# Kernel tuning notes

Measured on AMD Instinct MI355X. Metric: run time of the kernel, lower is better.

## Reference

```python
import jax, jax.numpy as jnp
import numpy as np

DILATION = 3
HC_MULT = 4
HIDDEN_DIM = 32
ENGRAM_DIM = 32
KERNEL_SIZE = 4
EPS = 1.1920929e-07  # torch RMSNorm default eps=None -> finfo(fp32).eps


def rmsnorm(x, w):
    # x: [..., C], w broadcastable to x
    ms = jnp.mean(x * x, axis=-1, keepdims=True)
    return x * jax.lax.rsqrt(ms + EPS) * w


def setup_inputs() -> dict:
    key = jax.random.key(0)
    ks = jax.random.split(key, 12)
    B, T = 16, 8192
    s = 0.05
    return {
        "embeddings": jax.random.normal(ks[0], (B, T, ENGRAM_DIM), jnp.float32),
        "hidden_states": jax.random.normal(ks[1], (B, T, HC_MULT, HIDDEN_DIM), jnp.float32),
        "Wv": jax.random.normal(ks[2], (HIDDEN_DIM, ENGRAM_DIM), jnp.float32) * s,
        "bv": jax.random.normal(ks[3], (HIDDEN_DIM,), jnp.float32) * s,
        "Wk": jax.random.normal(ks[4], (HC_MULT, HIDDEN_DIM, ENGRAM_DIM), jnp.float32) * s,
        "bk": jax.random.normal(ks[5], (HC_MULT, HIDDEN_DIM), jnp.float32) * s,
        "n1_w": jnp.ones((HC_MULT, HIDDEN_DIM), jnp.float32),
        "n2_w": jnp.ones((HC_MULT, HIDDEN_DIM), jnp.float32),
        "cn_w": jnp.ones((HC_MULT, HIDDEN_DIM), jnp.float32),
        "conv_w": jax.random.normal(ks[6], (HC_MULT * HIDDEN_DIM, 1, KERNEL_SIZE), jnp.float32) * s,
    }


def reference(embeddings, hidden_states, Wv, bv, Wk, bk, n1_w, n2_w, cn_w, conv_w):
    B, T, G, C = hidden_states.shape
    # per-branch key projection: [B,T,G,C]
    key = jnp.einsum("btd,gcd->btgc", embeddings, Wk) + bk
    normed_key = rmsnorm(key, n1_w)                    # [B,T,G,C]
    normed_query = rmsnorm(hidden_states, n2_w)        # [B,T,G,C]
    gate = jnp.sum(normed_key * normed_query, axis=-1) / np.sqrt(C)  # [B,T,G]
    gate = jnp.sqrt(jnp.maximum(jnp.abs(gate), 1e-6)) * jnp.sign(gate)
    gate = jax.nn.sigmoid(gate)[..., None]             # [B,T,G,1]
    value = (embeddings @ Wv.T + bv)[:, :, None, :]    # [B,T,1,C]
    gated = gate * value                               # [B,T,G,C]
    # per-branch RMSNorm then concat channels
    x_norm = rmsnorm(gated, cn_w).reshape(B, T, G * C)
    x_bct = jnp.transpose(x_norm, (0, 2, 1))           # [B, G*C, T]
    pad = (KERNEL_SIZE - 1) * DILATION                 # causal left pad = 9
    y_bct = jax.lax.conv_general_dilated(
        x_bct, conv_w,
        window_strides=(1,), padding=[(pad, 0)],
        rhs_dilation=(DILATION,),
        dimension_numbers=("NCH", "OIH", "NCH"),
        feature_group_count=G * C,
    )
    y_bct = jax.nn.silu(y_bct)
    conv_out = jnp.transpose(y_bct, (0, 2, 1)).reshape(B, T, G, C)
    return gated + conv_out
```

## Files before the change

kernel.cpp:

```cpp
#include <hip/hip_runtime.h>
#include <hip/hip_fp16.h>

#define TT    64
#define HALO  9
#define NTOK  73
#define XSTR  132
#define VSTR  36
#define EPS   1.1920929e-07f

typedef __attribute__((ext_vector_type(8))) _Float16 f16x8;
typedef __attribute__((ext_vector_type(4))) float f32x4;

template<int CTRL>
__device__ __forceinline__ float dpp_add(float x) {
    int y = __builtin_amdgcn_update_dpp(0, __float_as_int(x), CTRL, 0xF, 0xF, true);
    return x + __int_as_float(y);
}
__device__ __forceinline__ float redsum16(float x) {
    x = dpp_add<0x128>(x);
    x = dpp_add<0x124>(x);
    x = dpp_add<0x122>(x);
    x = dpp_add<0x121>(x);
    return x;
}

__device__ __forceinline__ float fast_rcp(float x) {
    return __builtin_amdgcn_rcpf(x);
}

extern "C" __global__ __launch_bounds__(320, 3)
void engram_fused(const float* __restrict__ emb,
                  const float* __restrict__ hid,
                  const float* __restrict__ Wv,
                  const float* __restrict__ bv,
                  const float* __restrict__ Wk,
                  const float* __restrict__ bk,
                  const float* __restrict__ n1w,
                  const float* __restrict__ n2w,
                  const float* __restrict__ cnw,
                  const float* __restrict__ cw,
                  float* __restrict__ out)
{
    __shared__ __align__(16) __half s_xn[NTOK * XSTR];
    __shared__ __align__(16) float  s_val[TT * VSTR];
    __shared__ float  s_gate[TT * 4];

    const int tid  = threadIdx.x;
    const int b    = blockIdx.x >> 7;
    const int tile = blockIdx.x & 127;
    const int t0   = tile * TT;

    const int wv  = tid >> 6;
    const int ln  = tid & 63;
    const int l15 = ln & 15;
    const int q   = ln >> 4;
    const int ibase = wv * 16 + q * 4;


    float2 q2[4][4];
    float  okm[4];
    #pragma unroll
    for (int r = 0; r < 4; ++r) {
        int t = t0 - HALO + ibase + r;
        okm[r] = (t >= 0 && t < 8192) ? 1.f : 0.f;
        int tc = t < 0 ? 0 : (t > 8191 ? 8191 : t);
        const float2* qp = (const float2*)&hid[(size_t)((b << 13) + tc) * 128];
        #pragma unroll
        for (int g = 0; g < 4; ++g) q2[r][g] = qp[g * 16 + l15];
    }

    float4 f0, f1;
    float amask;
    {
        const int tA = t0 - HALO + wv * 16 + l15;
        amask = (tA >= 0 && tA < 8192) ? 1.f : 0.f;
        const int tAc = tA < 0 ? 0 : (tA > 8191 ? 8191 : tA);
        const float4* p = (const float4*)&emb[(size_t)((b << 13) + tAc) * 32 + q * 8];
        f0 = p[0];
        f1 = p[1];
    }

    const float2 bv2 = ((const float2*)bv)[l15];
    float2 bk2[4], wn1[4], wn2[4], wcn[4];
    #pragma unroll
    for (int g = 0; g < 4; ++g) {
        bk2[g] = ((const float2*)(bk  + g * 32))[l15];
        wn1[g] = ((const float2*)(n1w + g * 32))[l15];
        wn2[g] = ((const float2*)(n2w + g * 32))[l15];
        wcn[g] = ((const float2*)(cnw + g * 32))[l15];
    }

    f16x8 a;
    a[0] = (_Float16)(amask * f0.x); a[1] = (_Float16)(amask * f0.y);
    a[2] = (_Float16)(amask * f0.z); a[3] = (_Float16)(amask * f0.w);
    a[4] = (_Float16)(amask * f1.x); a[5] = (_Float16)(amask * f1.y);
    a[6] = (_Float16)(amask * f1.z); a[7] = (_Float16)(amask * f1.w);

    f32x4 D[10];
    #pragma unroll
    for (int nt = 0; nt < 10; ++nt) {
        const int e = nt & 1, p = nt >> 1;
        const int ch = 2 * l15 + e;
        const float* wrow = (p == 0) ? &Wv[ch * 32] : &Wk[((p - 1) * 32 + ch) * 32];
        float4 w0 = ((const float4*)wrow)[q * 2];
        float4 w1 = ((const float4*)wrow)[q * 2 + 1];
        f16x8 bf;
        bf[0] = (_Float16)w0.x; bf[1] = (_Float16)w0.y;
        bf[2] = (_Float16)w0.z; bf[3] = (_Float16)w0.w;
        bf[4] = (_Float16)w1.x; bf[5] = (_Float16)w1.y;
        bf[6] = (_Float16)w1.z; bf[7] = (_Float16)w1.w;
        const float bias = (p == 0) ? (e ? bv2.y : bv2.x)
                                    : (e ? bk2[p - 1].y : bk2[p - 1].x);
        f32x4 c = {bias, bias, bias, bias};
        D[nt] = __builtin_amdgcn_mfma_f32_16x16x32_f16(a, bf, c, 0, 0, 0);
    }

    #pragma unroll
    for (int r = 0; r < 4; ++r) {
        const int i = ibase + r;
        const float V0 = D[0][r], V1 = D[1][r];
        float msv = redsum16(V0 * V0 + V1 * V1);
        float gs[4];
        float xn[4][2];
        #pragma unroll
        for (int g = 0; g < 4; ++g) {
            const float K0 = D[2 + 2 * g][r], K1 = D[3 + 2 * g][r];
            const float q0 = q2[r][g].x * okm[r], q1 = q2[r][g].y * okm[r];
            float msk = redsum16(K0 * K0 + K1 * K1);
            float msq = redsum16(q0 * q0 + q1 * q1);
            float dr  = redsum16(K0 * wn1[g].x * q0 * wn2[g].x
                               + K1 * wn1[g].y * q1 * wn2[g].y);
            float rk = rsqrtf(msk * (1.f / 32.f) + EPS);
            float rq = rsqrtf(msq * (1.f / 32.f) + EPS);
            float dot = dr * rk * rq * 0.17677669529663689f;
            float sa = sqrtf(fmaxf(fabsf(dot), 1e-6f));
            float gate = fast_rcp(1.f + __expf(-copysignf(sa, dot)));
            gs[g] = gate;
            float sc = gate * rsqrtf(gate * gate * msv * (1.f / 32.f) + EPS);
            xn[g][0] = sc * V0 * wcn[g].x;
            xn[g][1] = sc * V1 * wcn[g].y;
        }
        if (i < NTOK) {
            #pragma unroll
            for (int g = 0; g < 4; ++g) {
                __half2 h2 = __floats2half2_rn(okm[r] * xn[g][0], okm[r] * xn[g][1]);
                *(__half2*)&s_xn[i * XSTR + g * 32 + 2 * l15] = h2;
            }
            if (i >= HALO) {
                const int j = i - HALO;
                *(float2*)&s_val[j * VSTR + 2 * l15] = make_float2(V0, V1);
                if (l15 < 4) {
                    float gsel = (l15 == 0) ? gs[0] : (l15 == 1) ? gs[1]
                               : (l15 == 2) ? gs[2] : gs[3];
                    s_gate[j * 4 + l15] = gsel;
                }
            }
        }
    }
    __syncthreads();

    const float4* cw4p = (const float4*)cw;
    for (int idx = tid; idx < TT * 32; idx += 320) {
        const int j  = idx >> 5;
        const int c4 = (idx & 31) << 2;
        float4 w0 = cw4p[c4 + 0];
        float4 w1 = cw4p[c4 + 1];
        float4 w2 = cw4p[c4 + 2];
        float4 w3 = cw4p[c4 + 3];
        float y0 = 0.f, y1 = 0.f, y2 = 0.f, y3 = 0.f;
        #pragma unroll
        for (int k = 0; k < 4; ++k) {
            const __half2* xp = (const __half2*)&s_xn[(j + 3 * k) * XSTR + c4];
            float2 a01 = __half22float2(xp[0]);
            float2 a23 = __half22float2(xp[1]);
            const float wk0 = (k == 0) ? w0.x : (k == 1) ? w0.y : (k == 2) ? w0.z : w0.w;
            const float wk1 = (k == 0) ? w1.x : (k == 1) ? w1.y : (k == 2) ? w1.z : w1.w;
            const float wk2 = (k == 0) ? w2.x : (k == 1) ? w2.y : (k == 2) ? w2.z : w2.w;
            const float wk3 = (k == 0) ? w3.x : (k == 1) ? w3.y : (k == 2) ? w3.z : w3.w;
            y0 = fmaf(a01.x, wk0, y0);
            y1 = fmaf(a01.y, wk1, y1);
            y2 = fmaf(a23.x, wk2, y2);
            y3 = fmaf(a23.y, wk3, y3);
        }
        const float g  = s_gate[j * 4 + (c4 >> 5)];
        const f32x4 v  = *(const f32x4*)&s_val[j * VSTR + (c4 & 31)];
        float4 o;
        o.x = g * v[0] + y0 * fast_rcp(1.f + __expf(-y0));
        o.y = g * v[1] + y1 * fast_rcp(1.f + __expf(-y1));
        o.z = g * v[2] + y2 * fast_rcp(1.f + __expf(-y2));
        o.w = g * v[3] + y3 * fast_rcp(1.f + __expf(-y3));
        *(float4*)&out[(size_t)((b << 13) + t0 + j) * 128 + c4] = o;
    }
}

extern "C" void kernel_launch(void* const* d_in, const int* in_sizes, int n_in,
                              void* d_out, int out_size, void* d_ws, size_t ws_size,
                              hipStream_t stream) {
    const float* emb = (const float*)d_in[0];
    const float* hid = (const float*)d_in[1];
    const float* Wv  = (const float*)d_in[2];
    const float* bvp = (const float*)d_in[3];
    const float* Wk  = (const float*)d_in[4];
    const float* bkp = (const float*)d_in[5];
    const float* n1  = (const float*)d_in[6];
    const float* n2  = (const float*)d_in[7];
    const float* cn  = (const float*)d_in[8];
    const float* cwp = (const float*)d_in[9];
    float* out = (float*)d_out;

    dim3 grid(16 * 128);
    dim3 block(320);
    engram_fused<<<grid, block, 0, stream>>>(emb, hid, Wv, bvp, Wk, bkp, n1, n2, cn, cwp, out);
}
```

Baseline: 191.2 us.

## Keep gate and value in registers; compute conv epilogue in MFMA lane layout

Drops the shared-memory staging of the value vector and per-token gates. The conv+SiLU epilogue now runs in the same thread/token mapping as the MFMA accumulators, so gate and value are read straight from registers. Launch bounds are raised to target six blocks per CU. The cost is that some lanes (halo rows) sit idle in the epilogue, outputs become float2 stores instead of float4, and register pressure under the tighter launch bound may cause spills.

Measured after the change: 235.9 us. +23.4%, slower.

```diff
diff --git a/kernel.cpp b/kernel.cpp
--- a/kernel.cpp
+++ b/kernel.cpp
@@ -5,7 +5,6 @@
 #define HALO  9
 #define NTOK  73
 #define XSTR  132
-#define VSTR  36
 #define EPS   1.1920929e-07f
 
 typedef __attribute__((ext_vector_type(8))) _Float16 f16x8;
@@ -28,7 +27,7 @@
     return __builtin_amdgcn_rcpf(x);
 }
 
-extern "C" __global__ __launch_bounds__(320, 3)
+extern "C" __global__ __launch_bounds__(320, 6)
 void engram_fused(const float* __restrict__ emb,
                   const float* __restrict__ hid,
                   const float* __restrict__ Wv,
@@ -42,8 +41,6 @@
                   float* __restrict__ out)
 {
     __shared__ __align__(16) __half s_xn[NTOK * XSTR];
-    __shared__ __align__(16) float  s_val[TT * VSTR];
-    __shared__ float  s_gate[TT * 4];
 
     const int tid  = threadIdx.x;
     const int b    = blockIdx.x >> 7;
@@ -115,12 +112,12 @@
         D[nt] = __builtin_amdgcn_mfma_f32_16x16x32_f16(a, bf, c, 0, 0, 0);
     }
 
+    float gs4[4][4];
     #pragma unroll
     for (int r = 0; r < 4; ++r) {
         const int i = ibase + r;
         const float V0 = D[0][r], V1 = D[1][r];
         float msv = redsum16(V0 * V0 + V1 * V1);
-        float gs[4];
         float xn[4][2];
         #pragma unroll
         for (int g = 0; g < 4; ++g) {
@@ -135,7 +132,7 @@
             float dot = dr * rk * rq * 0.17677669529663689f;
             float sa = sqrtf(fmaxf(fabsf(dot), 1e-6f));
             float gate = fast_rcp(1.f + __expf(-copysignf(sa, dot)));
-            gs[g] = gate;
+            gs4[r][g] = gate;
             float sc = gate * rsqrtf(gate * gate * msv * (1.f / 32.f) + EPS);
             xn[g][0] = sc * V0 * wcn[g].x;
             xn[g][1] = sc * V1 * wcn[g].y;
@@ -146,50 +143,40 @@
                 __half2 h2 = __floats2half2_rn(okm[r] * xn[g][0], okm[r] * xn[g][1]);
                 *(__half2*)&s_xn[i * XSTR + g * 32 + 2 * l15] = h2;
             }
-            if (i >= HALO) {
-                const int j = i - HALO;
-                *(float2*)&s_val[j * VSTR + 2 * l15] = make_float2(V0, V1);
-                if (l15 < 4) {
-                    float gsel = (l15 == 0) ? gs[0] : (l15 == 1) ? gs[1]
-                               : (l15 == 2) ? gs[2] : gs[3];
-                    s_gate[j * 4 + l15] = gsel;
+        }
+    }
+    __syncthreads();
+
+    const float4* cw4p = (const float4*)cw;
+    #pragma unroll
+    for (int g = 0; g < 4; ++g) {
+        const int ch = g * 32 + 2 * l15;
+        const float4 wA = cw4p[ch];
+        const float4 wB = cw4p[ch + 1];
+        #pragma unroll
+        for (int r = 0; r < 4; ++r) {
+            const int i = ibase + r;
+            const int j = i - HALO;
+            if (i >= HALO && i < NTOK) {
+                float y0 = 0.f, y1 = 0.f;
+                #pragma unroll
+                for (int k = 0; k < 4; ++k) {
+                    float2 x = __half22float2(
+                        *(const __half2*)&s_xn[(j + 3 * k) * XSTR + ch]);
+                    const float wk0 = (k == 0) ? wA.x : (k == 1) ? wA.y
+                                    : (k == 2) ? wA.z : wA.w;
+                    const float wk1 = (k == 0) ? wB.x : (k == 1) ? wB.y
+                                    : (k == 2) ? wB.z : wB.w;
+                    y0 = fmaf(x.x, wk0, y0);
+                    y1 = fmaf(x.y, wk1, y1);
                 }
+                const float gg = gs4[r][g];
+                float2 o;
+                o.x = gg * D[0][r] + y0 * fast_rcp(1.f + __expf(-y0));
+                o.y = gg * D[1][r] + y1 * fast_rcp(1.f + __expf(-y1));
+                *(float2*)&out[(size_t)((b << 13) + t0 + j) * 128 + ch] = o;
             }
         }
-    }
-    __syncthreads();
-
-    const float4* cw4p = (const float4*)cw;
-    for (int idx = tid; idx < TT * 32; idx += 320) {
-        const int j  = idx >> 5;
-        const int c4 = (idx & 31) << 2;
-        float4 w0 = cw4p[c4 + 0];
-        float4 w1 = cw4p[c4 + 1];
-        float4 w2 = cw4p[c4 + 2];
-        float4 w3 = cw4p[c4 + 3];
-        float y0 = 0.f, y1 = 0.f, y2 = 0.f, y3 = 0.f;
-        #pragma unroll
-        for (int k = 0; k < 4; ++k) {
-            const __half2* xp = (const __half2*)&s_xn[(j + 3 * k) * XSTR + c4];
-            float2 a01 = __half22float2(xp[0]);
-            float2 a23 = __half22float2(xp[1]);
-            const float wk0 = (k == 0) ? w0.x : (k == 1) ? w0.y : (k == 2) ? w0.z : w0.w;
-            const float wk1 = (k == 0) ? w1.x : (k == 1) ? w1.y : (k == 2) ? w1.z : w1.w;
-            const float wk2 = (k == 0) ? w2.x : (k == 1) ? w2.y : (k == 2) ? w2.z : w2.w;
-            const float wk3 = (k == 0) ? w3.x : (k == 1) ? w3.y : (k == 2) ? w3.z : w3.w;
-            y0 = fmaf(a01.x, wk0, y0);
-            y1 = fmaf(a01.y, wk1, y1);
-            y2 = fmaf(a23.x, wk2, y2);
-            y3 = fmaf(a23.y, wk3, y3);
-        }
-        const float g  = s_gate[j * 4 + (c4 >> 5)];
-        const f32x4 v  = *(const f32x4*)&s_val[j * VSTR + (c4 & 31)];
-        float4 o;
-        o.x = g * v[0] + y0 * fast_rcp(1.f + __expf(-y0));
-        o.y = g * v[1] + y1 * fast_rcp(1.f + __expf(-y1));
-        o.z = g * v[2] + y2 * fast_rcp(1.f + __expf(-y2));
-        o.w = g * v[3] + y3 * fast_rcp(1.f + __expf(-y3));
-        *(float4*)&out[(size_t)((b << 13) + t0 + j) * 128 + c4] = o;
     }
 }
 
```

## Process two time tiles per block and prefetch next tile's hidden states

Applied to the files above, without the earlier changes.

Each block now handles two consecutive 64-token sub-tiles in a loop, with the grid halved. The hidden-state loads for the second sub-tile are issued before the first sub-tile's conv/output phase, so their latency overlaps that work. It also amortises per-block setup (bias and norm weight loads) over two tiles. In exchange it adds register pressure from a second q2 buffer, an extra barrier, and fewer blocks in flight, which can lower occupancy and the latency hiding it provides.

Result: slower. 225.8 us (+18.1%).

```diff
diff --git a/kernel.cpp b/kernel.cpp
--- a/kernel.cpp
+++ b/kernel.cpp
@@ -2,6 +2,7 @@
 #include <hip/hip_fp16.h>
 
 #define TT    64
+#define NSUB  2
 #define HALO  9
 #define NTOK  73
 #define XSTR  132
@@ -46,39 +47,14 @@
     __shared__ float  s_gate[TT * 4];
 
     const int tid  = threadIdx.x;
-    const int b    = blockIdx.x >> 7;
-    const int tile = blockIdx.x & 127;
-    const int t0   = tile * TT;
+    const int b    = blockIdx.x >> 6;
+    const int tp   = blockIdx.x & 63;
 
     const int wv  = tid >> 6;
     const int ln  = tid & 63;
     const int l15 = ln & 15;
     const int q   = ln >> 4;
     const int ibase = wv * 16 + q * 4;
-
-
-    float2 q2[4][4];
-    float  okm[4];
-    #pragma unroll
-    for (int r = 0; r < 4; ++r) {
-        int t = t0 - HALO + ibase + r;
-        okm[r] = (t >= 0 && t < 8192) ? 1.f : 0.f;
-        int tc = t < 0 ? 0 : (t > 8191 ? 8191 : t);
-        const float2* qp = (const float2*)&hid[(size_t)((b << 13) + tc) * 128];
-        #pragma unroll
-        for (int g = 0; g < 4; ++g) q2[r][g] = qp[g * 16 + l15];
-    }
-
-    float4 f0, f1;
-    float amask;
-    {
-        const int tA = t0 - HALO + wv * 16 + l15;
-        amask = (tA >= 0 && tA < 8192) ? 1.f : 0.f;
-        const int tAc = tA < 0 ? 0 : (tA > 8191 ? 8191 : tA);
-        const float4* p = (const float4*)&emb[(size_t)((b << 13) + tAc) * 32 + q * 8];
-        f0 = p[0];
-        f1 = p[1];
-    }
 
     const float2 bv2 = ((const float2*)bv)[l15];
     float2 bk2[4], wn1[4], wn2[4], wcn[4];
@@ -90,106 +66,162 @@
         wcn[g] = ((const float2*)(cnw + g * 32))[l15];
     }
 
-    f16x8 a;
-    a[0] = (_Float16)(amask * f0.x); a[1] = (_Float16)(amask * f0.y);
-    a[2] = (_Float16)(amask * f0.z); a[3] = (_Float16)(amask * f0.w);
-    a[4] = (_Float16)(amask * f1.x); a[5] = (_Float16)(amask * f1.y);
-    a[6] = (_Float16)(amask * f1.z); a[7] = (_Float16)(amask * f1.w);
-
-    f32x4 D[10];
+    float2 q2[4][4];
+    float  okm[4];
+    {
+        const int t0 = tp * (TT * NSUB);
+        #pragma unroll
+        for (int r = 0; r < 4; ++r) {
+            int t = t0 - HALO + ibase + r;
+            okm[r] = (t >= 0 && t < 8192) ? 1.f : 0.f;
+            int tc = t < 0 ? 0 : (t > 8191 ? 8191 : t);
+            const float2* qp = (const float2*)&hid[(size_t)((b << 13) + tc) * 128];
+            #pragma unroll
+            for (int g = 0; g < 4; ++g) q2[r][g] = qp[g * 16 + l15];
+        }
+    }
+
     #pragma unroll
-    for (int nt = 0; nt < 10; ++nt) {
-        const int e = nt & 1, p = nt >> 1;
-        const int ch = 2 * l15 + e;
-        const float* wrow = (p == 0) ? &Wv[ch * 32] : &Wk[((p - 1) * 32 + ch) * 32];
-        float4 w0 = ((const float4*)wrow)[q * 2];
-        float4 w1 = ((const float4*)wrow)[q * 2 + 1];
-        f16x8 bf;
-        bf[0] = (_Float16)w0.x; bf[1] = (_Float16)w0.y;
-        bf[2] = (_Float16)w0.z; bf[3] = (_Float16)w0.w;
-        bf[4] = (_Float16)w1.x; bf[5] = (_Float16)w1.y;
-        bf[6] = (_Float16)w1.z; bf[7] = (_Float16)w1.w;
-        const float bias = (p == 0) ? (e ? bv2.y : bv2.x)
-                                    : (e ? bk2[p - 1].y : bk2[p - 1].x);
-        f32x4 c = {bias, bias, bias, bias};
-        D[nt] = __builtin_amdgcn_mfma_f32_16x16x32_f16(a, bf, c, 0, 0, 0);
-    }
-
-    #pragma unroll
-    for (int r = 0; r < 4; ++r) {
-        const int i = ibase + r;
-        const float V0 = D[0][r], V1 = D[1][r];
-        float msv = redsum16(V0 * V0 + V1 * V1);
-        float gs[4];
-        float xn[4][2];
+    for (int sub = 0; sub < NSUB; ++sub) {
+        const int t0 = tp * (TT * NSUB) + sub * TT;
+
+        float4 f0, f1;
+        float amask;
+        {
+            const int tA = t0 - HALO + wv * 16 + l15;
+            amask = (tA >= 0 && tA < 8192) ? 1.f : 0.f;
+            const int tAc = tA < 0 ? 0 : (tA > 8191 ? 8191 : tA);
+            const float4* p = (const float4*)&emb[(size_t)((b << 13) + tAc) * 32 + q * 8];
+            f0 = p[0];
+            f1 = p[1];
+        }
+
+        f16x8 a;
+        a[0] = (_Float16)(amask * f0.x); a[1] = (_Float16)(amask * f0.y);
+        a[2] = (_Float16)(amask * f0.z); a[3] = (_Float16)(amask * f0.w);
+        a[4] = (_Float16)(amask * f1.x); a[5] = (_Float16)(amask * f1.y);
+        a[6] = (_Float16)(amask * f1.z); a[7] = (_Float16)(amask * f1.w);
+
+        f32x4 D[10];
         #pragma unroll
-        for (int g = 0; g < 4; ++g) {
-            const float K0 = D[2 + 2 * g][r], K1 = D[3 + 2 * g][r];
-            const float q0 = q2[r][g].x * okm[r], q1 = q2[r][g].y * okm[r];
-            float msk = redsum16(K0 * K0 + K1 * K1);
-            float msq = redsum16(q0 * q0 + q1 * q1);
-            float dr  = redsum16(K0 * wn1[g].x * q0 * wn2[g].x
-                               + K1 * wn1[g].y * q1 * wn2[g].y);
-            float rk = rsqrtf(msk * (1.f / 32.f) + EPS);
-            float rq = rsqrtf(msq * (1.f / 32.f) + EPS);
-            float dot = dr * rk * rq * 0.17677669529663689f;
-            float sa = sqrtf(fmaxf(fabsf(dot), 1e-6f));
-            float gate = fast_rcp(1.f + __expf(-copysignf(sa, dot)));
-            gs[g] = gate;
-            float sc = gate * rsqrtf(gate * gate * msv * (1.f / 32.f) + EPS);
-            xn[g][0] = sc * V0 * wcn[g].x;
-            xn[g][1] = sc * V1 * wcn[g].y;
-        }
-        if (i < NTOK) {
+        for (int nt = 0; nt < 10; ++nt) {
+            const int e = nt & 1, p = nt >> 1;
+            const int ch = 2 * l15 + e;
+            const float* wrow = (p == 0) ? &Wv[ch * 32] : &Wk[((p - 1) * 32 + ch) * 32];
+            float4 w0 = ((const float4*)wrow)[q * 2];
+            float4 w1 = ((const float4*)wrow)[q * 2 + 1];
+            f16x8 bf;
+            bf[0] = (_Float16)w0.x; bf[1] = (_Float16)w0.y;
+            bf[2] = (_Float16)w0.z; bf[3] = (_Float16)w0.w;
+            bf[4] = (_Float16)w1.x; bf[5] = (_Float16)w1.y;
+            bf[6] = (_Float16)w1.z; bf[7] = (_Float16)w1.w;
+            const float bias = (p == 0) ? (e ? bv2.y : bv2.x)
+                                        : (e ? bk2[p - 1].y : bk2[p - 1].x);
+            f32x4 c = {bias, bias, bias, bias};
+            D[nt] = __builtin_amdgcn_mfma_f32_16x16x32_f16(a, bf, c, 0, 0, 0);
+        }
+
+        #pragma unroll
+        for (int r = 0; r < 4; ++r) {
+            const int i = ibase + r;
+            const float V0 = D[0][r], V1 = D[1][r];
+            float msv = redsum16(V0 * V0 + V1 * V1);
+            float gs[4];
+            float xn[4][2];
             #pragma unroll
             for (int g = 0; g < 4; ++g) {
-                __half2 h2 = __floats2half2_rn(okm[r] * xn[g][0], okm[r] * xn[g][1]);
-                *(__half2*)&s_xn[i * XSTR + g * 32 + 2 * l15] = h2;
-            }
-            if (i >= HALO) {
-                const int j = i - HALO;
-                *(float2*)&s_val[j * VSTR + 2 * l15] = make_float2(V0, V1);
-                if (l15 < 4) {
-                    float gsel = (l15 == 0) ? gs[0] : (l15 == 1) ? gs[1]
-                               : (l15 == 2) ? gs[2] : gs[3];
-                    s_gate[j * 4 + l15] = gsel;
+                const float K0 = D[2 + 2 * g][r], K1 = D[3 + 2 * g][r];
+                const float q0 = q2[r][g].x * okm[r], q1 = q2[r][g].y * okm[r];
+                float msk = redsum16(K0 * K0 + K1 * K1);
+                float msq = redsum16(q0 * q0 + q1 * q1);
+                float dr  = redsum16(K0 * wn1[g].x * q0 * wn2[g].x
+                                   + K1 * wn1[g].y * q1 * wn2[g].y);
+                float rk = rsqrtf(msk * (1.f / 32.f) + EPS);
+                float rq = rsqrtf(msq * (1.f / 32.f) + EPS);
+                float dot = dr * rk * rq * 0.17677669529663689f;
+                float sa = sqrtf(fmaxf(fabsf(dot), 1e-6f));
+                float gate = fast_rcp(1.f + __expf(-copysignf(sa, dot)));
+                gs[g] = gate;
+                float sc = gate * rsqrtf(gate * gate * msv * (1.f / 32.f) + EPS);
+                xn[g][0] = sc * V0 * wcn[g].x;
+                xn[g][1] = sc * V1 * wcn[g].y;
+            }
+            if (i < NTOK) {
+                #pragma unroll
+                for (int g = 0; g < 4; ++g) {
+                    __half2 h2 = __floats2half2_rn(okm[r] * xn[g][0], okm[r] * xn[g][1]);
+                    *(__half2*)&s_xn[i * XSTR + g * 32 + 2 * l15] = h2;
                 }
-            }
-        }
-    }
-    __syncthreads();
-
-    const float4* cw4p = (const float4*)cw;
-    for (int idx = tid; idx < TT * 32; idx += 320) {
-        const int j  = idx >> 5;
-        const int c4 = (idx & 31) << 2;
-        float4 w0 = cw4p[c4 + 0];
-        float4 w1 = cw4p[c4 + 1];
-        float4 w2 = cw4p[c4 + 2];
-        float4 w3 = cw4p[c4 + 3];
-        float y0 = 0.f, y1 = 0.f, y2 = 0.f, y3 = 0.f;
-        #pragma unroll
-        for (int k = 0; k < 4; ++k) {
-            const __half2* xp = (const __half2*)&s_xn[(j + 3 * k) * XSTR + c4];
-            float2 a01 = __half22float2(xp[0]);
-            float2 a23 = __half22float2(xp[1]);
-            const float wk0 = (k == 0) ? w0.x : (k == 1) ? w0.y : (k == 2) ? w0.z : w0.w;
-            const float wk1 = (k == 0) ? w1.x : (k == 1) ? w1.y : (k == 2) ? w1.z : w1.w;
-            const float wk2 = (k == 0) ? w2.x : (k == 1) ? w2.y : (k == 2) ? w2.z : w2.w;
-            const float wk3 = (k == 0) ? w3.x : (k == 1) ? w3.y : (k == 2) ? w3.z : w3.w;
-            y0 = fmaf(a01.x, wk0, y0);
-            y1 = fmaf(a01.y, wk1, y1);
-            y2 = fmaf(a23.x, wk2, y2);
-            y3 = fmaf(a23.y, wk3, y3);
-        }
-        const float g  = s_gate[j * 4 + (c4 >> 5)];
-        const f32x4 v  = *(const f32x4*)&s_val[j * VSTR + (c4 & 31)];
-        float4 o;
-        o.x = g * v[0] + y0 * fast_rcp(1.f + __expf(-y0));
-        o.y = g * v[1] + y1 * fast_rcp(1.f + __expf(-y1));
-        o.z = g * v[2] + y2 * fast_rcp(1.f + __expf(-y2));
-        o.w = g * v[3] + y3 * fast_rcp(1.f + __expf(-y3));
-        *(float4*)&out[(size_t)((b << 13) + t0 + j) * 128 + c4] = o;
+                if (i >= HALO) {
+                    const int j = i - HALO;
+                    *(float2*)&s_val[j * VSTR + 2 * l15] = make_float2(V0, V1);
+                    if (l15 < 4) {
+                        float gsel = (l15 == 0) ? gs[0] : (l15 == 1) ? gs[1]
+                                   : (l15 == 2) ? gs[2] : gs[3];
+                        s_gate[j * 4 + l15] = gsel;
+                    }
+                }
+            }
+        }
+        __syncthreads();
+
+        float2 q2n[4][4];
+        float  okmn[4];
+        if (sub + 1 < NSUB) {
+            const int t0n = t0 + TT;
+            #pragma unroll
+            for (int r = 0; r < 4; ++r) {
+                int t = t0n - HALO + ibase + r;
+                okmn[r] = (t >= 0 && t < 8192) ? 1.f : 0.f;
+                int tc = t < 0 ? 0 : (t > 8191 ? 8191 : t);
+                const float2* qp = (const float2*)&hid[(size_t)((b << 13) + tc) * 128];
+                #pragma unroll
+                for (int g = 0; g < 4; ++g) q2n[r][g] = qp[g * 16 + l15];
+            }
+        }
+
+        const float4* cw4p = (const float4*)cw;
+        for (int idx = tid; idx < TT * 32; idx += 320) {
+            const int j  = idx >> 5;
+            const int c4 = (idx & 31) << 2;
+            float4 w0 = cw4p[c4 + 0];
+            float4 w1 = cw4p[c4 + 1];
+            float4 w2 = cw4p[c4 + 2];
+            float4 w3 = cw4p[c4 + 3];
+            float y0 = 0.f, y1 = 0.f, y2 = 0.f, y3 = 0.f;
+            #pragma unroll
+            for (int k = 0; k < 4; ++k) {
+                const __half2* xp = (const __half2*)&s_xn[(j + 3 * k) * XSTR + c4];
+                float2 a01 = __half22float2(xp[0]);
+                float2 a23 = __half22float2(xp[1]);
+                const float wk0 = (k == 0) ? w0.x : (k == 1) ? w0.y : (k == 2) ? w0.z : w0.w;
+                const float wk1 = (k == 0) ? w1.x : (k == 1) ? w1.y : (k == 2) ? w1.z : w1.w;
+                const float wk2 = (k == 0) ? w2.x : (k == 1) ? w2.y : (k == 2) ? w2.z : w2.w;
+                const float wk3 = (k == 0) ? w3.x : (k == 1) ? w3.y : (k == 2) ? w3.z : w3.w;
+                y0 = fmaf(a01.x, wk0, y0);
+                y1 = fmaf(a01.y, wk1, y1);
+                y2 = fmaf(a23.x, wk2, y2);
+                y3 = fmaf(a23.y, wk3, y3);
+            }
+            const float g  = s_gate[j * 4 + (c4 >> 5)];
+            const f32x4 v  = *(const f32x4*)&s_val[j * VSTR + (c4 & 31)];
+            float4 o;
+            o.x = g * v[0] + y0 * fast_rcp(1.f + __expf(-y0));
+            o.y = g * v[1] + y1 * fast_rcp(1.f + __expf(-y1));
+            o.z = g * v[2] + y2 * fast_rcp(1.f + __expf(-y2));
+            o.w = g * v[3] + y3 * fast_rcp(1.f + __expf(-y3));
+            *(float4*)&out[(size_t)((b << 13) + t0 + j) * 128 + c4] = o;
+        }
+
+        if (sub + 1 < NSUB) {
+            #pragma unroll
+            for (int r = 0; r < 4; ++r) {
+                okm[r] = okmn[r];
+                #pragma unroll
+                for (int g = 0; g < 4; ++g) q2[r][g] = q2n[r][g];
+            }
+            __syncthreads();
+        }
     }
 }
 
@@ -208,7 +240,7 @@
     const float* cwp = (const float*)d_in[9];
     float* out = (float*)d_out;
 
-    dim3 grid(16 * 128);
+    dim3 grid(16 * 64);
     dim3 block(320);
     engram_fused<<<grid, block, 0, stream>>>(emb, hid, Wv, bvp, Wk, bkp, n1, n2, cn, cwp, out);
 }
```

## Split fused kernel into norm and conv kernels via workspace

Applied to the files above, without the earlier changes.

Splits the single fused kernel into two. The first computes projections, gates and normalized activations per token and writes them to a global workspace (fp16 xn, fp32 value and gate). The second runs the dilated causal depthwise conv plus SiLU per element, reading the halo from global memory. This removes the 9-token halo recompute and the shared-memory staging, at the cost of an extra global round trip of about 50 MB and a second launch. The fused kernel is kept as a fallback when the workspace is too small.

After: 181.2 us. 1.05x faster.

```diff
diff --git a/kernel.cpp b/kernel.cpp
--- a/kernel.cpp
+++ b/kernel.cpp
@@ -26,6 +26,170 @@
 
 __device__ __forceinline__ float fast_rcp(float x) {
     return __builtin_amdgcn_rcpf(x);
+}
+
+extern "C" __global__ __launch_bounds__(256)
+void engram_norm(const float* __restrict__ emb,
+                 const float* __restrict__ hid,
+                 const float* __restrict__ Wv,
+                 const float* __restrict__ bv,
+                 const float* __restrict__ Wk,
+                 const float* __restrict__ bk,
+                 const float* __restrict__ n1w,
+                 const float* __restrict__ n2w,
+                 const float* __restrict__ cnw,
+                 __half* __restrict__ xn_out,
+                 float* __restrict__ val_out,
+                 float* __restrict__ gate_out)
+{
+    const int tid  = threadIdx.x;
+    const int b    = blockIdx.x >> 7;
+    const int tile = blockIdx.x & 127;
+    const int t0   = tile * 64;
+
+    const int wv  = tid >> 6;
+    const int ln  = tid & 63;
+    const int l15 = ln & 15;
+    const int q   = ln >> 4;
+    const int tw  = t0 + wv * 16;
+
+    float2 q2[4][4];
+    #pragma unroll
+    for (int r = 0; r < 4; ++r) {
+        const int t = tw + q * 4 + r;
+        const float2* qp = (const float2*)&hid[(size_t)((b << 13) + t) * 128];
+        #pragma unroll
+        for (int g = 0; g < 4; ++g) q2[r][g] = qp[g * 16 + l15];
+    }
+
+    float4 f0, f1;
+    {
+        const float4* p = (const float4*)&emb[(size_t)((b << 13) + tw + l15) * 32 + q * 8];
+        f0 = p[0];
+        f1 = p[1];
+    }
+
+    const float2 bv2 = ((const float2*)bv)[l15];
+    float2 bk2[4], wn1[4], wn2[4], wcn[4];
+    #pragma unroll
+    for (int g = 0; g < 4; ++g) {
+        bk2[g] = ((const float2*)(bk  + g * 32))[l15];
+        wn1[g] = ((const float2*)(n1w + g * 32))[l15];
+        wn2[g] = ((const float2*)(n2w + g * 32))[l15];
+        wcn[g] = ((const float2*)(cnw + g * 32))[l15];
+    }
+
+    f16x8 a;
+    a[0] = (_Float16)f0.x; a[1] = (_Float16)f0.y;
+    a[2] = (_Float16)f0.z; a[3] = (_Float16)f0.w;
+    a[4] = (_Float16)f1.x; a[5] = (_Float16)f1.y;
+    a[6] = (_Float16)f1.z; a[7] = (_Float16)f1.w;
+
+    f32x4 D[10];
+    #pragma unroll
+    for (int nt = 0; nt < 10; ++nt) {
+        const int e = nt & 1, p = nt >> 1;
+        const int ch = 2 * l15 + e;
+        const float* wrow = (p == 0) ? &Wv[ch * 32] : &Wk[((p - 1) * 32 + ch) * 32];
+        float4 w0 = ((const float4*)wrow)[q * 2];
+        float4 w1 = ((const float4*)wrow)[q * 2 + 1];
+        f16x8 bf;
+        bf[0] = (_Float16)w0.x; bf[1] = (_Float16)w0.y;
+        bf[2] = (_Float16)w0.z; bf[3] = (_Float16)w0.w;
+        bf[4] = (_Float16)w1.x; bf[5] = (_Float16)w1.y;
+        bf[6] = (_Float16)w1.z; bf[7] = (_Float16)w1.w;
+        const float bias = (p == 0) ? (e ? bv2.y : bv2.x)
+                                    : (e ? bk2[p - 1].y : bk2[p - 1].x);
+        f32x4 c = {bias, bias, bias, bias};
+        D[nt] = __builtin_amdgcn_mfma_f32_16x16x32_f16(a, bf, c, 0, 0, 0);
+    }
+
+    #pragma unroll
+    for (int r = 0; r < 4; ++r) {
+        const int ti = tw + q * 4 + r;
+        const float V0 = D[0][r], V1 = D[1][r];
+        float msv = redsum16(V0 * V0 + V1 * V1);
+        float gs[4];
+        float xnv[4][2];
+        #pragma unroll
+        for (int g = 0; g < 4; ++g) {
+            const float K0 = D[2 + 2 * g][r], K1v = D[3 + 2 * g][r];
+            const float q0 = q2[r][g].x, q1 = q2[r][g].y;
+            float msk = redsum16(K0 * K0 + K1v * K1v);
+            float msq = redsum16(q0 * q0 + q1 * q1);
+            float dr  = redsum16(K0 * wn1[g].x * q0 * wn2[g].x
+                               + K1v * wn1[g].y * q1 * wn2[g].y);
+            float rk = rsqrtf(msk * (1.f / 32.f) + EPS);
+            float rq = rsqrtf(msq * (1.f / 32.f) + EPS);
+            float dot = dr * rk * rq * 0.17677669529663689f;
+            float sa = sqrtf(fmaxf(fabsf(dot), 1e-6f));
+            float gate = fast_rcp(1.f + __expf(-copysignf(sa, dot)));
+            gs[g] = gate;
+            float sc = gate * rsqrtf(gate * gate * msv * (1.f / 32.f) + EPS);
+            xnv[g][0] = sc * V0 * wcn[g].x;
+            xnv[g][1] = sc * V1 * wcn[g].y;
+        }
+        __half* xrow = xn_out + (size_t)((b << 13) + ti) * 128;
+        #pragma unroll
+        for (int g = 0; g < 4; ++g) {
+            *(__half2*)&xrow[g * 32 + 2 * l15] = __floats2half2_rn(xnv[g][0], xnv[g][1]);
+        }
+        *(float2*)&val_out[(size_t)((b << 13) + ti) * 32 + 2 * l15] = make_float2(V0, V1);
+        if (l15 < 4) {
+            float gsel = (l15 == 0) ? gs[0] : (l15 == 1) ? gs[1]
+                       : (l15 == 2) ? gs[2] : gs[3];
+            gate_out[(size_t)((b << 13) + ti) * 4 + l15] = gsel;
+        }
+    }
+}
+
+extern "C" __global__ __launch_bounds__(256)
+void engram_conv(const __half* __restrict__ xn,
+                 const float* __restrict__ val,
+                 const float* __restrict__ gate,
+                 const float* __restrict__ cw,
+                 float* __restrict__ out)
+{
+    const int gid = blockIdx.x * 256 + threadIdx.x;
+    const int c4i = gid & 31;
+    const int c4  = c4i << 2;
+    const int t   = (gid >> 5) & 8191;
+    const int b   = gid >> 18;
+    const int g   = c4 >> 5;
+
+    const float4* cw4p = (const float4*)cw;
+    const float4 w0 = cw4p[c4 + 0];
+    const float4 w1 = cw4p[c4 + 1];
+    const float4 w2 = cw4p[c4 + 2];
+    const float4 w3 = cw4p[c4 + 3];
+
+    const size_t row = (size_t)((b << 13) + t);
+    float y0 = 0.f, y1 = 0.f, y2 = 0.f, y3 = 0.f;
+    #pragma unroll
+    for (int k = 0; k < 4; ++k) {
+        const int tp  = t - HALO + 3 * k;
+        const float m = (tp >= 0) ? 1.f : 0.f;
+        const int tpc = tp < 0 ? 0 : tp;
+        const __half2* xp = (const __half2*)&xn[(size_t)((b << 13) + tpc) * 128 + c4];
+        float2 a01 = __half22float2(xp[0]);
+        float2 a23 = __half22float2(xp[1]);
+        const float wk0 = (k == 0) ? w0.x : (k == 1) ? w0.y : (k == 2) ? w0.z : w0.w;
+        const float wk1 = (k == 0) ? w1.x : (k == 1) ? w1.y : (k == 2) ? w1.z : w1.w;
+        const float wk2 = (k == 0) ? w2.x : (k == 1) ? w2.y : (k == 2) ? w2.z : w2.w;
+        const float wk3 = (k == 0) ? w3.x : (k == 1) ? w3.y : (k == 2) ? w3.z : w3.w;
+        y0 = fmaf(m * a01.x, wk0, y0);
+        y1 = fmaf(m * a01.y, wk1, y1);
+        y2 = fmaf(m * a23.x, wk2, y2);
+        y3 = fmaf(m * a23.y, wk3, y3);
+    }
+    const float gg = gate[row * 4 + g];
+    const f32x4 v  = *(const f32x4*)&val[row * 32 + (c4 & 31)];
+    float4 o;
+    o.x = gg * v[0] + y0 * fast_rcp(1.f + __expf(-y0));
+    o.y = gg * v[1] + y1 * fast_rcp(1.f + __expf(-y1));
+    o.z = gg * v[2] + y2 * fast_rcp(1.f + __expf(-y2));
+    o.w = gg * v[3] + y3 * fast_rcp(1.f + __expf(-y3));
+    *(float4*)&out[row * 128 + c4] = o;
 }
 
 extern "C" __global__ __launch_bounds__(320, 3)
@@ -56,7 +220,6 @@
     const int q   = ln >> 4;
     const int ibase = wv * 16 + q * 4;
 
-
     float2 q2[4][4];
     float  okm[4];
     #pragma unroll
@@ -121,15 +284,15 @@
         const float V0 = D[0][r], V1 = D[1][r];
         float msv = redsum16(V0 * V0 + V1 * V1);
         float gs[4];
-        float xn[4][2];
+        float xnv[4][2];
         #pragma unroll
         for (int g = 0; g < 4; ++g) {
-            const float K0 = D[2 + 2 * g][r], K1 = D[3 + 2 * g][r];
+            const float K0 = D[2 + 2 * g][r], K1v = D[3 + 2 * g][r];
             const float q0 = q2[r][g].x * okm[r], q1 = q2[r][g].y * okm[r];
-            float msk = redsum16(K0 * K0 + K1 * K1);
+            float msk = redsum16(K0 * K0 + K1v * K1v);
             float msq = redsum16(q0 * q0 + q1 * q1);
             float dr  = redsum16(K0 * wn1[g].x * q0 * wn2[g].x
-                               + K1 * wn1[g].y * q1 * wn2[g].y);
+                               + K1v * wn1[g].y * q1 * wn2[g].y);
             float rk = rsqrtf(msk * (1.f / 32.f) + EPS);
             float rq = rsqrtf(msq * (1.f / 32.f) + EPS);
             float dot = dr * rk * rq * 0.17677669529663689f;
@@ -137,13 +300,13 @@
             float gate = fast_rcp(1.f + __expf(-copysignf(sa, dot)));
             gs[g] = gate;
             float sc = gate * rsqrtf(gate * gate * msv * (1.f / 32.f) + EPS);
-            xn[g][0] = sc * V0 * wcn[g].x;
-            xn[g][1] = sc * V1 * wcn[g].y;
+            xnv[g][0] = sc * V0 * wcn[g].x;
+            xnv[g][1] = sc * V1 * wcn[g].y;
         }
         if (i < NTOK) {
             #pragma unroll
             for (int g = 0; g < 4; ++g) {
-                __half2 h2 = __floats2half2_rn(okm[r] * xn[g][0], okm[r] * xn[g][1]);
+                __half2 h2 = __floats2half2_rn(okm[r] * xnv[g][0], okm[r] * xnv[g][1]);
                 *(__half2*)&s_xn[i * XSTR + g * 32 + 2 * l15] = h2;
             }
             if (i >= HALO) {
@@ -208,7 +371,21 @@
     const float* cwp = (const float*)d_in[9];
     float* out = (float*)d_out;
 
-    dim3 grid(16 * 128);
-    dim3 block(320);
-    engram_fused<<<grid, block, 0, stream>>>(emb, hid, Wv, bvp, Wk, bkp, n1, n2, cn, cwp, out);
-}
+    const size_t xn_bytes   = (size_t)16 * 8192 * 128 * sizeof(__half);
+    const size_t val_bytes  = (size_t)16 * 8192 * 32 * sizeof(float);
+    const size_t gate_bytes = (size_t)16 * 8192 * 4 * sizeof(float);
+    const size_t need = xn_bytes + val_bytes + gate_bytes;
+
+    if (d_ws != nullptr && ws_size >= need) {
+        __half* xn  = (__half*)d_ws;
+        float* val  = (float*)((char*)d_ws + xn_bytes);
+        float* gate = (float*)((char*)d_ws + xn_bytes + val_bytes);
+        engram_norm<<<dim3(16 * 128), dim3(256), 0, stream>>>(
+            emb, hid, Wv, bvp, Wk, bkp, n1, n2, cn, xn, val, gate);
+        engram_conv<<<dim3(16 * 8192 * 32 / 256), dim3(256), 0, stream>>>(
+            xn, val, gate, cwp, out);
+    } else {
+        engram_fused<<<dim3(16 * 128), dim3(320), 0, stream>>>(
+            emb, hid, Wv, bvp, Wk, bkp, n1, n2, cn, cwp, out);
+    }
+}
```
